# Optimization experiments

Measured on AMD Instinct MI355X. Metric: run time of the kernel, lower is better.

## Reference

```python
import jax, jax.numpy as jnp
import numpy as np

B, D_IN, HID, DIM, M = 4096, 128, 200, 256, 32
SIGMA, OMEGA = 1.0, 1.7
LB, UB = 0.0, 1.0


def setup_inputs() -> dict:
    key = jax.random.key(0)
    ks = jax.random.split(key, 9)
    s = lambda d: 1.0 / jnp.sqrt(jnp.float32(d))
    return {
        "x": jax.random.normal(ks[0], (B, D_IN), jnp.float32),
        "b": jax.random.uniform(ks[1], (B, M), jnp.float32),
        "W1": jax.random.normal(ks[2], (D_IN, HID), jnp.float32) * s(D_IN),
        "b1": jnp.zeros((HID,), jnp.float32),
        "W2": jax.random.normal(ks[3], (HID, HID), jnp.float32) * s(HID),
        "b2": jnp.zeros((HID,), jnp.float32),
        "W3": jax.random.normal(ks[4], (HID, DIM), jnp.float32) * s(HID),
        "b3": jnp.zeros((DIM,), jnp.float32),
        "A": jax.random.normal(ks[5], (M, DIM), jnp.float32) * s(DIM),
        "step": 1000,
        "n_iter": 100,
    }


def reference(x, b, W1, b1, W2, b2, W3, b3, A, step, n_iter):
    # --- MLP: Dense(200) -> relu -> Dense(200) -> relu -> Dense(dim) ---
    h = jax.nn.relu(x @ W1 + b1)
    h = jax.nn.relu(h @ W2 + b2)
    y = h @ W3 + b3  # [B, DIM]

    # schedule = linear_schedule(0.0, 0.0, ...) -> alpha == 0.0 always
    alpha = jnp.float32(0.0)

    # --- projection onto {z : A z = b, LB <= z <= UB} via relaxed
    # Douglas-Rachford / SOR fixed-point iteration (sigma/omega) ---
    AAt_inv = jnp.linalg.inv(A @ A.T + 1e-6 * jnp.eye(M, dtype=A.dtype))

    def p_aff(z):  # affine equality projection, z: [B, DIM]
        r = z @ A.T - b            # [B, M] residual
        return z - (r @ AAt_inv) @ A

    def p_box(z):
        return jnp.clip(z, LB, UB)

    def body(z, _):
        u = p_aff(z)
        v = p_box(2.0 * u - z)     # reflection then box projection
        z = z + SIGMA * OMEGA * (v - u)
        return z, None

    z0 = y  # project.get_init(x): initialize fixed point at MLP output
    z_final, _ = jax.lax.scan(body, z0, None, length=n_iter)
    proj = p_aff(z_final)

    # interpolation between raw MLP output and projection (alpha == 0)
    out = alpha * y + (1.0 - alpha) * proj
    return out
```

## Files before the change

kernel.cpp:

```cpp
#include <hip/hip_runtime.h>
#include <hip/hip_bf16.h>

typedef float    f4v    __attribute__((ext_vector_type(4)));
typedef short    short8 __attribute__((ext_vector_type(8)));
typedef unsigned u2v    __attribute__((ext_vector_type(2)));

constexpr int Bn = 4096, D_IN = 128, HID = 200, DIM = 256, TR = 16;

__global__ __launch_bounds__(1024) void k_prep(const float* __restrict__ A,
                                               float* __restrict__ KAT) {
  __shared__ float As[32 * 256];
  __shared__ float Gm[32 * 68];
  __shared__ float ck[32];
  const int t = threadIdx.x;

  for (int i = t; i < 2048; i += 1024) ((f4v*)As)[i] = ((const f4v*)A)[i];

  {
    const int gi = t >> 5, gj = t & 31;
    f4v acc = {0.f, 0.f, 0.f, 0.f};
    const f4v* ai = (const f4v*)(A + gi * 256);
    const f4v* aj = (const f4v*)(A + gj * 256);
    for (int k = 0; k < 64; ++k) acc += ai[k] * aj[k];
    float s = acc[0] + acc[1] + acc[2] + acc[3];
    if (gi == gj) s += 1e-6f;
    Gm[gi * 68 + gj] = s;
    Gm[gi * 68 + 32 + gj] = (gi == gj) ? 1.f : 0.f;
  }
  __syncthreads();

  for (int k = 0; k < 32; ++k) {
    if (t < 32) ck[t] = Gm[t * 68 + k];
    __syncthreads();
    float ip = 1.f / ck[k];
    if (t < 64) Gm[k * 68 + t] *= ip;
    __syncthreads();
    for (int idx = t; idx < 2048; idx += 1024) {
      int i = idx >> 6, j = idx & 63;
      if (i != k) Gm[i * 68 + j] = fmaf(-ck[i], Gm[k * 68 + j], Gm[i * 68 + j]);
    }
    __syncthreads();
  }

  {
    const int j = t & 255, mq = t >> 8;
    float colA[32];
    #pragma unroll
    for (int n = 0; n < 32; ++n) colA[n] = As[n * 256 + j];
    float res[8];
    #pragma unroll
    for (int mm = 0; mm < 8; ++mm) {
      const float* g = &Gm[(8 * mq + mm) * 68 + 32];
      float s = 0.f;
      #pragma unroll
      for (int n = 0; n < 32; ++n) s = fmaf(g[n], colA[n], s);
      res[mm] = s;
    }
    f4v v0 = {res[0], res[1], res[2], res[3]};
    f4v v1 = {res[4], res[5], res[6], res[7]};
    *(f4v*)&KAT[j * 32 + 8 * mq] = v0;
    *(f4v*)&KAT[j * 32 + 8 * mq + 4] = v1;
  }
}

__device__ inline unsigned cvt2(float x, float y) {
  union { __hip_bfloat162 h; unsigned u; } c;
  c.h = __float22bfloat162_rn(float2{x, y});
  return c.u;
}
__device__ inline void split_pair(float x, float y, unsigned& hp, unsigned& lp) {
  hp = cvt2(x, y);
  float hx = __uint_as_float(hp << 16);
  float hy = __uint_as_float(hp & 0xffff0000u);
  lp = cvt2(x - hx, y - hy);
}
union S8U { unsigned u[4]; short8 s; };
__device__ inline void split8(const float v[8], short8& hi, short8& lo) {
  S8U h, l;
  #pragma unroll
  for (int d = 0; d < 4; ++d) split_pair(v[2 * d], v[2 * d + 1], h.u[d], l.u[d]);
  hi = h.s; lo = l.s;
}
__device__ inline f4v mfma16(short8 a, short8 b, f4v c) {
  return __builtin_amdgcn_mfma_f32_16x16x32_bf16(a, b, c, 0, 0, 0);
}

__global__ __launch_bounds__(512, 1) void k_main(
    const float* __restrict__ x,  const float* __restrict__ bmat,
    const float* __restrict__ W1, const float* __restrict__ b1,
    const float* __restrict__ W2, const float* __restrict__ b2,
    const float* __restrict__ W3, const float* __restrict__ b3,
    const float* __restrict__ A,  const float* __restrict__ KAT,
    const int* __restrict__ n_iter_p, float* __restrict__ out) {

  __shared__ float ubuf[8768];
  __shared__ __align__(16) unsigned zfrag[4096];
  __shared__ __align__(16) unsigned rfrag[1024];

  const int t = threadIdx.x;
  const int lane = t & 63, wv = t >> 6, quad = lane >> 4, l15 = lane & 15;
  const int row0 = blockIdx.x * TR;

  float* xs = ubuf;
  float* h1 = ubuf + 2112;
  float* h2 = ubuf + 5440;
  float* ys = ubuf;

  if (t < 512) {
    int r = t >> 5, c4 = t & 31;
    *(f4v*)&xs[r * 132 + 4 * c4] = *(const f4v*)&x[(size_t)(row0 + r) * 128 + 4 * c4];
  }
  __syncthreads();

  {
    const int rg = wv, oc = lane;
    const bool g3 = (oc < 8);
    float acc[4][2];

    #pragma unroll
    for (int oi = 0; oi < 4; ++oi) { acc[oi][0] = 0.f; acc[oi][1] = 0.f; }
    for (int k4 = 0; k4 < 32; ++k4) {
      f4v xv0 = *(const f4v*)&xs[(2 * rg + 0) * 132 + 4 * k4];
      f4v xv1 = *(const f4v*)&xs[(2 * rg + 1) * 132 + 4 * k4];
      #pragma unroll
      for (int kk = 0; kk < 4; ++kk) {
        const float* wr = W1 + (4 * k4 + kk) * 200 + oc;
        float w0 = wr[0], w1c = wr[64], w2c = wr[128];
        float w3c = g3 ? wr[192] : 0.f;
        acc[0][0] = fmaf(xv0[kk], w0, acc[0][0]);  acc[0][1] = fmaf(xv1[kk], w0, acc[0][1]);
        acc[1][0] = fmaf(xv0[kk], w1c, acc[1][0]); acc[1][1] = fmaf(xv1[kk], w1c, acc[1][1]);
        acc[2][0] = fmaf(xv0[kk], w2c, acc[2][0]); acc[2][1] = fmaf(xv1[kk], w2c, acc[2][1]);
        acc[3][0] = fmaf(xv0[kk], w3c, acc[3][0]); acc[3][1] = fmaf(xv1[kk], w3c, acc[3][1]);
      }
    }
    #pragma unroll
    for (int oi = 0; oi < 4; ++oi) {
      if (oi == 3 && !g3) continue;
      float bb = b1[oc + 64 * oi];
      h1[(2 * rg + 0) * 208 + oc + 64 * oi] = fmaxf(acc[oi][0] + bb, 0.f);
      h1[(2 * rg + 1) * 208 + oc + 64 * oi] = fmaxf(acc[oi][1] + bb, 0.f);
    }
    __syncthreads();

    #pragma unroll
    for (int oi = 0; oi < 4; ++oi) { acc[oi][0] = 0.f; acc[oi][1] = 0.f; }
    for (int k4 = 0; k4 < 50; ++k4) {
      f4v xv0 = *(const f4v*)&h1[(2 * rg + 0) * 208 + 4 * k4];
      f4v xv1 = *(const f4v*)&h1[(2 * rg + 1) * 208 + 4 * k4];
      #pragma unroll
      for (int kk = 0; kk < 4; ++kk) {
        const float* wr = W2 + (4 * k4 + kk) * 200 + oc;
        float w0 = wr[0], w1c = wr[64], w2c = wr[128];
        float w3c = g3 ? wr[192] : 0.f;
        acc[0][0] = fmaf(xv0[kk], w0, acc[0][0]);  acc[0][1] = fmaf(xv1[kk], w0, acc[0][1]);
        acc[1][0] = fmaf(xv0[kk], w1c, acc[1][0]); acc[1][1] = fmaf(xv1[kk], w1c, acc[1][1]);
        acc[2][0] = fmaf(xv0[kk], w2c, acc[2][0]); acc[2][1] = fmaf(xv1[kk], w2c, acc[2][1]);
        acc[3][0] = fmaf(xv0[kk], w3c, acc[3][0]); acc[3][1] = fmaf(xv1[kk], w3c, acc[3][1]);
      }
    }
    #pragma unroll
    for (int oi = 0; oi < 4; ++oi) {
      if (oi == 3 && !g3) continue;
      float bb = b2[oc + 64 * oi];
      h2[(2 * rg + 0) * 208 + oc + 64 * oi] = fmaxf(acc[oi][0] + bb, 0.f);
      h2[(2 * rg + 1) * 208 + oc + 64 * oi] = fmaxf(acc[oi][1] + bb, 0.f);
    }
    __syncthreads();

    #pragma unroll
    for (int oi = 0; oi < 4; ++oi) { acc[oi][0] = 0.f; acc[oi][1] = 0.f; }
    for (int k4 = 0; k4 < 50; ++k4) {
      f4v xv0 = *(const f4v*)&h2[(2 * rg + 0) * 208 + 4 * k4];
      f4v xv1 = *(const f4v*)&h2[(2 * rg + 1) * 208 + 4 * k4];
      #pragma unroll
      for (int kk = 0; kk < 4; ++kk) {
        const float* wr = W3 + (4 * k4 + kk) * 256 + oc;
        float w0 = wr[0], w1c = wr[64], w2c = wr[128], w3c = wr[192];
        acc[0][0] = fmaf(xv0[kk], w0, acc[0][0]);  acc[0][1] = fmaf(xv1[kk], w0, acc[0][1]);
        acc[1][0] = fmaf(xv0[kk], w1c, acc[1][0]); acc[1][1] = fmaf(xv1[kk], w1c, acc[1][1]);
        acc[2][0] = fmaf(xv0[kk], w2c, acc[2][0]); acc[2][1] = fmaf(xv1[kk], w2c, acc[2][1]);
        acc[3][0] = fmaf(xv0[kk], w3c, acc[3][0]); acc[3][1] = fmaf(xv1[kk], w3c, acc[3][1]);
      }
    }
    __syncthreads();
    #pragma unroll
    for (int oi = 0; oi < 4; ++oi) {
      float bb = b3[oc + 64 * oi];
      ys[(2 * rg + 0) * 260 + oc + 64 * oi] = acc[oi][0] + bb;
      ys[(2 * rg + 1) * 260 + oc + 64 * oi] = acc[oi][1] + bb;
    }
  }
  __syncthreads();

  const int T  = wv & 1;
  const int kh = wv >> 1;

  short8 aah[4], aal[4];
  f4v binit = {0.f, 0.f, 0.f, 0.f};
  if (wv < 4) {
    #pragma unroll
    for (int s = 0; s < 4; ++s) {
      const float* ap = A + (size_t)(l15 + 16 * T) * 256 + 128 * kh + 32 * s + 8 * quad;
      float v[8];
      #pragma unroll
      for (int j = 0; j < 8; ++j) v[j] = ap[j];
      split8(v, aah[s], aal[s]);
    }
    if (wv < 2) {
      f4v bv = *(const f4v*)&bmat[(size_t)(row0 + l15) * 32 + 16 * T + 4 * quad];
      binit = -bv;
    }
  }

  short8 kanh[2], kanl[2];
  #pragma unroll
  for (int u = 0; u < 2; ++u) {
    const int U = 2 * wv + u;
    const float* kp = KAT + (size_t)(16 * U + l15) * 32 + 8 * quad;
    float v[8];
    #pragma unroll
    for (int j = 0; j < 8; ++j) v[j] = kp[j];
    split8(v, kanh[u], kanl[u]);
  }

  int zoff[2];
  #pragma unroll
  for (int u = 0; u < 2; ++u) {
    const int U = 2 * wv + u;
    const int qp = 2 * (U & 1) + (quad >> 1);
    zoff[u] = (((U >> 3) * 4 + ((U >> 1) & 3)) * 2) * 256
              + qp * 64 + l15 * 4 + 2 * (quad & 1);
  }

  float zr[2][4];
  #pragma unroll
  for (int u = 0; u < 2; ++u) {
    const int U = 2 * wv + u;
    f4v yv = *(const f4v*)&ys[l15 * 260 + 16 * U + 4 * quad];
    #pragma unroll
    for (int r = 0; r < 4; ++r) zr[u][r] = yv[r];
    unsigned h0, l0, h1_, l1_;
    split_pair(zr[u][0], zr[u][1], h0, l0);
    split_pair(zr[u][2], zr[u][3], h1_, l1_);
    u2v hv; hv[0] = h0; hv[1] = h1_;
    u2v lv; lv[0] = l0; lv[1] = l1_;
    *(u2v*)&zfrag[zoff[u]] = hv;
    *(u2v*)&zfrag[zoff[u] + 256] = lv;
  }
  __syncthreads();

  const int niter = n_iter_p[0];

  for (int it = 0; it <= niter; ++it) {
    if (wv < 4) {
      short8 zfh[4], zfl[4];
      #pragma unroll
      for (int s = 0; s < 4; ++s) {
        zfh[s] = *(const short8*)&zfrag[((kh * 4 + s) * 2 + 0) * 256 + lane * 4];
        zfl[s] = *(const short8*)&zfrag[((kh * 4 + s) * 2 + 1) * 256 + lane * 4];
      }
      f4v c0 = binit, c1 = {0.f, 0.f, 0.f, 0.f};
      #pragma unroll
      for (int s = 0; s < 4; ++s) {
        f4v cc = (s & 1) ? c1 : c0;
        cc = mfma16(aah[s], zfh[s], cc);
        cc = mfma16(aal[s], zfh[s], cc);
        cc = mfma16(aah[s], zfl[s], cc);
        if (s & 1) c1 = cc; else c0 = cc;
      }
      f4v rA = c0 + c1;
      unsigned h0, l0, h1_, l1_;
      split_pair(rA[0], rA[1], h0, l0);
      split_pair(rA[2], rA[3], h1_, l1_);
      const int lanep = (2 * T + (quad >> 1)) * 16 + l15;
      const int rb = kh * 512 + lanep * 4 + 2 * (quad & 1);
      u2v hv; hv[0] = h0; hv[1] = h1_;
      u2v lv; lv[0] = l0; lv[1] = l1_;
      *(u2v*)&rfrag[rb] = hv;
      *(u2v*)&rfrag[rb + 256] = lv;
    }
    __syncthreads();

    const short8 rh0 = *(const short8*)&rfrag[0 * 256 + lane * 4];
    const short8 rl0 = *(const short8*)&rfrag[1 * 256 + lane * 4];
    const short8 rh1 = *(const short8*)&rfrag[2 * 256 + lane * 4];
    const short8 rl1 = *(const short8*)&rfrag[3 * 256 + lane * 4];
    f4v cB[2];
    #pragma unroll
    for (int u = 0; u < 2; ++u) {
      f4v cc = {0.f, 0.f, 0.f, 0.f};
      cc = mfma16(kanh[u], rh0, cc);
      cc = mfma16(kanl[u], rh0, cc);
      cc = mfma16(kanh[u], rl0, cc);
      cc = mfma16(kanh[u], rh1, cc);
      cc = mfma16(kanl[u], rh1, cc);
      cc = mfma16(kanh[u], rl1, cc);
      cB[u] = cc;
    }

    if (it < niter) {
      #pragma unroll
      for (int u = 0; u < 2; ++u) {
        #pragma unroll
        for (int r = 0; r < 4; ++r) {
          float z = zr[u][r], wvv = cB[u][r];
          float vv = fminf(fmaxf(z - 2.f * wvv, 0.f), 1.f);
          zr[u][r] = fmaf(1.7f, vv - z + wvv, z);
        }
        unsigned h0, l0, h1_, l1_;
        split_pair(zr[u][0], zr[u][1], h0, l0);
        split_pair(zr[u][2], zr[u][3], h1_, l1_);
        u2v hv; hv[0] = h0; hv[1] = h1_;
        u2v lv; lv[0] = l0; lv[1] = l1_;
        *(u2v*)&zfrag[zoff[u]] = hv;
        *(u2v*)&zfrag[zoff[u] + 256] = lv;
      }
      __syncthreads();
    } else {
      #pragma unroll
      for (int u = 0; u < 2; ++u) {
        const int U = 2 * wv + u;
        f4v ov;
        #pragma unroll
        for (int r = 0; r < 4; ++r) ov[r] = zr[u][r] - cB[u][r];
        *(f4v*)&out[(size_t)(row0 + l15) * 256 + 16 * U + 4 * quad] = ov;
      }
    }
  }
}

extern "C" void kernel_launch(void* const* d_in, const int* in_sizes, int n_in,
                              void* d_out, int out_size, void* d_ws, size_t ws_size,
                              hipStream_t stream) {
  const float* x    = (const float*)d_in[0];
  const float* bmat = (const float*)d_in[1];
  const float* W1   = (const float*)d_in[2];
  const float* b1   = (const float*)d_in[3];
  const float* W2   = (const float*)d_in[4];
  const float* b2   = (const float*)d_in[5];
  const float* W3   = (const float*)d_in[6];
  const float* b3   = (const float*)d_in[7];
  const float* A    = (const float*)d_in[8];
  const int*  n_it  = (const int*)d_in[10];
  float* KAT = (float*)d_ws;
  float* out = (float*)d_out;

  hipLaunchKernelGGL(k_prep, dim3(1), dim3(1024), 0, stream, A, KAT);
  hipLaunchKernelGGL(k_main, dim3(Bn / TR), dim3(512), 0, stream,
                     x, bmat, W1, b1, W2, b2, W3, b3, A, KAT, n_it, out);
}
```

Measured before the change: 254.5 us.

## Fuse Gram-inverse prep into main kernel and halve rows per block

Drops the separate single-block prep kernel. Each block now computes A·Aᵀ with split-bf16 MFMA, inverts it with a wave-level shuffle Gauss-Jordan, and builds A_invᵀ·A itself. The block shrinks to 256 threads handling 8 rows, with 2 blocks per CU, and each wave now owns 4 output tiles. This removes the serial one-block prep kernel and the launch gap before the main kernel, and raises the block count. In exchange, every block repeats the small prep work, and the 16-row MFMA tiles are half padding, which wastes matrix throughput during the iteration loop.

After: 462.2 us. +81.6%, slower.

```diff
diff --git a/kernel.cpp b/kernel.cpp
--- a/kernel.cpp
+++ b/kernel.cpp
@@ -5,63 +5,7 @@
 typedef short    short8 __attribute__((ext_vector_type(8)));
 typedef unsigned u2v    __attribute__((ext_vector_type(2)));
 
-constexpr int Bn = 4096, D_IN = 128, HID = 200, DIM = 256, TR = 16;
-
-__global__ __launch_bounds__(1024) void k_prep(const float* __restrict__ A,
-                                               float* __restrict__ KAT) {
-  __shared__ float As[32 * 256];
-  __shared__ float Gm[32 * 68];
-  __shared__ float ck[32];
-  const int t = threadIdx.x;
-
-  for (int i = t; i < 2048; i += 1024) ((f4v*)As)[i] = ((const f4v*)A)[i];
-
-  {
-    const int gi = t >> 5, gj = t & 31;
-    f4v acc = {0.f, 0.f, 0.f, 0.f};
-    const f4v* ai = (const f4v*)(A + gi * 256);
-    const f4v* aj = (const f4v*)(A + gj * 256);
-    for (int k = 0; k < 64; ++k) acc += ai[k] * aj[k];
-    float s = acc[0] + acc[1] + acc[2] + acc[3];
-    if (gi == gj) s += 1e-6f;
-    Gm[gi * 68 + gj] = s;
-    Gm[gi * 68 + 32 + gj] = (gi == gj) ? 1.f : 0.f;
-  }
-  __syncthreads();
-
-  for (int k = 0; k < 32; ++k) {
-    if (t < 32) ck[t] = Gm[t * 68 + k];
-    __syncthreads();
-    float ip = 1.f / ck[k];
-    if (t < 64) Gm[k * 68 + t] *= ip;
-    __syncthreads();
-    for (int idx = t; idx < 2048; idx += 1024) {
-      int i = idx >> 6, j = idx & 63;
-      if (i != k) Gm[i * 68 + j] = fmaf(-ck[i], Gm[k * 68 + j], Gm[i * 68 + j]);
-    }
-    __syncthreads();
-  }
-
-  {
-    const int j = t & 255, mq = t >> 8;
-    float colA[32];
-    #pragma unroll
-    for (int n = 0; n < 32; ++n) colA[n] = As[n * 256 + j];
-    float res[8];
-    #pragma unroll
-    for (int mm = 0; mm < 8; ++mm) {
-      const float* g = &Gm[(8 * mq + mm) * 68 + 32];
-      float s = 0.f;
-      #pragma unroll
-      for (int n = 0; n < 32; ++n) s = fmaf(g[n], colA[n], s);
-      res[mm] = s;
-    }
-    f4v v0 = {res[0], res[1], res[2], res[3]};
-    f4v v1 = {res[4], res[5], res[6], res[7]};
-    *(f4v*)&KAT[j * 32 + 8 * mq] = v0;
-    *(f4v*)&KAT[j * 32 + 8 * mq + 4] = v1;
-  }
-}
+constexpr int Bn = 4096, TR = 8;
 
 __device__ inline unsigned cvt2(float x, float y) {
   union { __hip_bfloat162 h; unsigned u; } c;
@@ -81,32 +25,136 @@
   for (int d = 0; d < 4; ++d) split_pair(v[2 * d], v[2 * d + 1], h.u[d], l.u[d]);
   hi = h.s; lo = l.s;
 }
+__device__ inline void split8p(const float* p, short8& hi, short8& lo) {
+  f4v a = *(const f4v*)p, b = *(const f4v*)(p + 4);
+  float v[8] = {a[0], a[1], a[2], a[3], b[0], b[1], b[2], b[3]};
+  split8(v, hi, lo);
+}
 __device__ inline f4v mfma16(short8 a, short8 b, f4v c) {
   return __builtin_amdgcn_mfma_f32_16x16x32_bf16(a, b, c, 0, 0, 0);
 }
-
-__global__ __launch_bounds__(512, 1) void k_main(
+__device__ __attribute__((always_inline)) inline f4v gdot8(
+    const short8 (&ah)[8], const short8 (&al)[8],
+    const short8 (&bh)[8], const short8 (&bl)[8]) {
+  f4v c = {0.f, 0.f, 0.f, 0.f};
+  #pragma unroll
+  for (int s = 0; s < 8; ++s) {
+    c = mfma16(ah[s], bh[s], c);
+    c = mfma16(al[s], bh[s], c);
+    c = mfma16(ah[s], bl[s], c);
+  }
+  return c;
+}
+
+__global__ __launch_bounds__(256, 2) void k_fused(
     const float* __restrict__ x,  const float* __restrict__ bmat,
     const float* __restrict__ W1, const float* __restrict__ b1,
     const float* __restrict__ W2, const float* __restrict__ b2,
     const float* __restrict__ W3, const float* __restrict__ b3,
-    const float* __restrict__ A,  const float* __restrict__ KAT,
-    const int* __restrict__ n_iter_p, float* __restrict__ out) {
-
-  __shared__ float ubuf[8768];
+    const float* __restrict__ A,  const int* __restrict__ n_iter_p,
+    float* __restrict__ out) {
+
+  __shared__ __align__(16) float    ubuf[8192];
   __shared__ __align__(16) unsigned zfrag[4096];
   __shared__ __align__(16) unsigned rfrag[1024];
 
   const int t = threadIdx.x;
   const int lane = t & 63, wv = t >> 6, quad = lane >> 4, l15 = lane & 15;
   const int row0 = blockIdx.x * TR;
+  const int T = wv & 1, kh = wv >> 1;
+
+  float* As    = ubuf;
+  float* Gm    = (float*)zfrag;
+  float* GinvL = (float*)rfrag;
+
+  for (int i = t; i < 2048; i += 256)
+    ((f4v*)As)[i] = ((const f4v*)A)[i];
+  __syncthreads();
+
+  {
+    short8 afh[2][8], afl[2][8];
+    #pragma unroll
+    for (int tt = 0; tt < 2; ++tt)
+      #pragma unroll
+      for (int s = 0; s < 8; ++s)
+        split8p(As + (l15 + 16 * tt) * 256 + 32 * s + 8 * quad,
+                afh[tt][s], afl[tt][s]);
+    f4v cg;
+    if      (wv == 0) cg = gdot8(afh[0], afl[0], afh[0], afl[0]);
+    else if (wv == 1) cg = gdot8(afh[1], afl[1], afh[0], afl[0]);
+    else if (wv == 2) cg = gdot8(afh[0], afl[0], afh[1], afl[1]);
+    else              cg = gdot8(afh[1], afl[1], afh[1], afl[1]);
+    #pragma unroll
+    for (int r = 0; r < 4; ++r) {
+      int gi = 16 * T + 4 * quad + r, gj = 16 * kh + l15;
+      Gm[gi * 68 + gj]      = cg[r] + (gi == gj ? 1e-6f : 0.f);
+      Gm[gi * 68 + 32 + gj] = (gi == gj) ? 1.f : 0.f;
+    }
+  }
+  __syncthreads();
+
+  if (wv == 0) {
+    float gcol[32];
+    #pragma unroll
+    for (int i = 0; i < 32; ++i) gcol[i] = Gm[i * 68 + lane];
+    #pragma unroll
+    for (int k = 0; k < 32; ++k) {
+      float ckk  = __shfl(gcol[k], k);
+      float ipiv = 1.f / ckk;
+      float pivj = gcol[k] * ipiv;
+      gcol[k] = pivj;
+      #pragma unroll
+      for (int i = 0; i < 32; ++i) {
+        if (i == k) continue;
+        float cki = __shfl(gcol[i], k);
+        gcol[i] = fmaf(-cki, pivj, gcol[i]);
+      }
+    }
+    if (lane >= 32) {
+      #pragma unroll
+      for (int i = 0; i < 32; ++i) GinvL[i * 32 + (lane - 32)] = gcol[i];
+    }
+  }
+  __syncthreads();
+
+  short8 kanh[4], kanl[4];
+  #pragma unroll
+  for (int u = 0; u < 4; ++u) {
+    const int n = 16 * (4 * wv + u) + l15;
+    float acc[8];
+    #pragma unroll
+    for (int j = 0; j < 8; ++j) acc[j] = 0.f;
+    for (int p = 0; p < 32; ++p) {
+      float av = As[p * 256 + n];
+      f4v g0 = *(const f4v*)&GinvL[p * 32 + 8 * quad];
+      f4v g1 = *(const f4v*)&GinvL[p * 32 + 8 * quad + 4];
+      acc[0] = fmaf(av, g0[0], acc[0]); acc[1] = fmaf(av, g0[1], acc[1]);
+      acc[2] = fmaf(av, g0[2], acc[2]); acc[3] = fmaf(av, g0[3], acc[3]);
+      acc[4] = fmaf(av, g1[0], acc[4]); acc[5] = fmaf(av, g1[1], acc[5]);
+      acc[6] = fmaf(av, g1[2], acc[6]); acc[7] = fmaf(av, g1[3], acc[7]);
+    }
+    split8(acc, kanh[u], kanl[u]);
+  }
+
+  short8 aah[4], aal[4];
+  #pragma unroll
+  for (int s = 0; s < 4; ++s)
+    split8p(As + (l15 + 16 * T) * 256 + 128 * kh + 32 * s + 8 * quad,
+            aah[s], aal[s]);
+
+  f4v binit = {0.f, 0.f, 0.f, 0.f};
+  if (wv < 2 && l15 < 8) {
+    f4v bv = *(const f4v*)&bmat[(size_t)(row0 + l15) * 32 + 16 * T + 4 * quad];
+    binit = -bv;
+  }
+  __syncthreads();
 
   float* xs = ubuf;
-  float* h1 = ubuf + 2112;
-  float* h2 = ubuf + 5440;
+  float* h1 = ubuf + 1056;
+  float* h2 = ubuf + 2720;
   float* ys = ubuf;
 
-  if (t < 512) {
+  {
     int r = t >> 5, c4 = t & 31;
     *(f4v*)&xs[r * 132 + 4 * c4] = *(const f4v*)&x[(size_t)(row0 + r) * 128 + 4 * c4];
   }
@@ -192,53 +240,22 @@
   }
   __syncthreads();
 
-  const int T  = wv & 1;
-  const int kh = wv >> 1;
-
-  short8 aah[4], aal[4];
-  f4v binit = {0.f, 0.f, 0.f, 0.f};
-  if (wv < 4) {
-    #pragma unroll
-    for (int s = 0; s < 4; ++s) {
-      const float* ap = A + (size_t)(l15 + 16 * T) * 256 + 128 * kh + 32 * s + 8 * quad;
-      float v[8];
-      #pragma unroll
-      for (int j = 0; j < 8; ++j) v[j] = ap[j];
-      split8(v, aah[s], aal[s]);
-    }
-    if (wv < 2) {
-      f4v bv = *(const f4v*)&bmat[(size_t)(row0 + l15) * 32 + 16 * T + 4 * quad];
-      binit = -bv;
-    }
-  }
-
-  short8 kanh[2], kanl[2];
-  #pragma unroll
-  for (int u = 0; u < 2; ++u) {
-    const int U = 2 * wv + u;
-    const float* kp = KAT + (size_t)(16 * U + l15) * 32 + 8 * quad;
-    float v[8];
-    #pragma unroll
-    for (int j = 0; j < 8; ++j) v[j] = kp[j];
-    split8(v, kanh[u], kanl[u]);
-  }
-
-  int zoff[2];
-  #pragma unroll
-  for (int u = 0; u < 2; ++u) {
-    const int U = 2 * wv + u;
+  int zoff[4];
+  #pragma unroll
+  for (int u = 0; u < 4; ++u) {
+    const int U = 4 * wv + u;
     const int qp = 2 * (U & 1) + (quad >> 1);
     zoff[u] = (((U >> 3) * 4 + ((U >> 1) & 3)) * 2) * 256
               + qp * 64 + l15 * 4 + 2 * (quad & 1);
   }
 
-  float zr[2][4];
-  #pragma unroll
-  for (int u = 0; u < 2; ++u) {
-    const int U = 2 * wv + u;
+  float zr[4][4];
+  #pragma unroll
+  for (int u = 0; u < 4; ++u) {
+    const int U = 4 * wv + u;
     f4v yv = *(const f4v*)&ys[l15 * 260 + 16 * U + 4 * quad];
     #pragma unroll
-    for (int r = 0; r < 4; ++r) zr[u][r] = yv[r];
+    for (int r = 0; r < 4; ++r) zr[u][r] = (l15 < 8) ? yv[r] : 0.f;
     unsigned h0, l0, h1_, l1_;
     split_pair(zr[u][0], zr[u][1], h0, l0);
     split_pair(zr[u][2], zr[u][3], h1_, l1_);
@@ -252,7 +269,7 @@
   const int niter = n_iter_p[0];
 
   for (int it = 0; it <= niter; ++it) {
-    if (wv < 4) {
+    {
       short8 zfh[4], zfl[4];
       #pragma unroll
       for (int s = 0; s < 4; ++s) {
@@ -285,9 +302,9 @@
     const short8 rl0 = *(const short8*)&rfrag[1 * 256 + lane * 4];
     const short8 rh1 = *(const short8*)&rfrag[2 * 256 + lane * 4];
     const short8 rl1 = *(const short8*)&rfrag[3 * 256 + lane * 4];
-    f4v cB[2];
-    #pragma unroll
-    for (int u = 0; u < 2; ++u) {
+    f4v cB[4];
+    #pragma unroll
+    for (int u = 0; u < 4; ++u) {
       f4v cc = {0.f, 0.f, 0.f, 0.f};
       cc = mfma16(kanh[u], rh0, cc);
       cc = mfma16(kanl[u], rh0, cc);
@@ -300,7 +317,7 @@
 
     if (it < niter) {
       #pragma unroll
-      for (int u = 0; u < 2; ++u) {
+      for (int u = 0; u < 4; ++u) {
         #pragma unroll
         for (int r = 0; r < 4; ++r) {
           float z = zr[u][r], wvv = cB[u][r];
@@ -317,13 +334,15 @@
       }
       __syncthreads();
     } else {
-      #pragma unroll
-      for (int u = 0; u < 2; ++u) {
-        const int U = 2 * wv + u;
-        f4v ov;
+      if (l15 < 8) {
         #pragma unroll
-        for (int r = 0; r < 4; ++r) ov[r] = zr[u][r] - cB[u][r];
-        *(f4v*)&out[(size_t)(row0 + l15) * 256 + 16 * U + 4 * quad] = ov;
+        for (int u = 0; u < 4; ++u) {
+          const int U = 4 * wv + u;
+          f4v ov;
+          #pragma unroll
+          for (int r = 0; r < 4; ++r) ov[r] = zr[u][r] - cB[u][r];
+          *(f4v*)&out[(size_t)(row0 + l15) * 256 + 16 * U + 4 * quad] = ov;
+        }
       }
     }
   }
@@ -342,10 +361,8 @@
   const float* b3   = (const float*)d_in[7];
   const float* A    = (const float*)d_in[8];
   const int*  n_it  = (const int*)d_in[10];
-  float* KAT = (float*)d_ws;
   float* out = (float*)d_out;
 
-  hipLaunchKernelGGL(k_prep, dim3(1), dim3(1024), 0, stream, A, KAT);
-  hipLaunchKernelGGL(k_main, dim3(Bn / TR), dim3(512), 0, stream,
-                     x, bmat, W1, b1, W2, b2, W3, b3, A, KAT, n_it, out);
-}
+  hipLaunchKernelGGL(k_fused, dim3(Bn / TR), dim3(256), 0, stream,
+                     x, bmat, W1, b1, W2, b2, W3, b3, A, n_it, out);
+}
```
